# Kernel optimization log

Hardware: AMD Instinct MI355X
Metric: run time of the kernel (lower is better)

The kernel has to match this reference:

```python
import jax, jax.numpy as jnp
import numpy as np
import math

B, NK, NQ = 8, 2048, 2048
DK = DQ = DV = 256
H = 1024


def setup_inputs() -> dict:
    key = jax.random.key(0)
    ks = jax.random.split(key, 11)
    def lin(kw, kb, fan_in, fan_out):
        bound = 1.0 / math.sqrt(fan_in)
        W = jax.random.uniform(kw, (fan_out, fan_in), minval=-bound, maxval=bound, dtype=jnp.float32)
        b = jax.random.uniform(kb, (fan_out,), minval=-bound, maxval=bound, dtype=jnp.float32)
        return W, b
    Wk_w, Wk_b = lin(ks[0], ks[1], DK, H)
    Wq_w, Wq_b = lin(ks[2], ks[3], DQ, H)
    Wv_w, Wv_b = lin(ks[4], ks[5], DV, H)
    lin_w, lin_b = lin(ks[6], ks[7], H, DV)
    KEY = jax.random.normal(ks[8], (B, NK, DK), dtype=jnp.float32)
    VALUE = jax.random.normal(ks[9], (B, NK, DV), dtype=jnp.float32)
    QUERY = jax.random.normal(ks[10], (B, NQ, DQ), dtype=jnp.float32)
    return {"KEY": KEY, "VALUE": VALUE, "QUERY": QUERY,
            "Wk_w": Wk_w, "Wk_b": Wk_b, "Wq_w": Wq_w, "Wq_b": Wq_b,
            "Wv_w": Wv_w, "Wv_b": Wv_b, "lin_w": lin_w, "lin_b": lin_b}


def reference(KEY, VALUE, QUERY, Wk_w, Wk_b, Wq_w, Wq_b, Wv_w, Wv_b, lin_w, lin_b):
    # Projections (dropout in eval mode == identity)
    Wk = KEY @ Wk_w.T + Wk_b      # [b, nk, h]
    Wq = QUERY @ Wq_w.T + Wq_b    # [b, nq, h]
    Wv = VALUE @ Wv_w.T + Wv_b    # [b, nk, h]
    scale = 1.0 / math.sqrt(Wq.shape[-1])
    # dist[b, i(key), k(query)]
    dist = jnp.einsum('bih,bkh->bik', Wk, Wq) * scale
    # softmax over the QUERY axis (dim=2), non-standard
    weights = jax.nn.softmax(dist, axis=2)
    # context[b, k(query), h]
    context = jnp.einsum('bik,bih->bkh', weights, Wv)
    res = context @ lin_w.T + lin_b  # [b, nq, input_v]
    return res
```

## Files before the change

### kernel.cpp

```cpp
#include <hip/hip_runtime.h>
#include <hip/hip_bf16.h>

using bf16 = __hip_bfloat16;
typedef __attribute__((ext_vector_type(8))) short s16x8;
typedef __attribute__((ext_vector_type(4))) float f32x4;

__device__ __forceinline__ void async_cp16(const void* g, void* lds) {
    __builtin_amdgcn_global_load_lds(
        (const __attribute__((address_space(1))) unsigned int*)g,
        (__attribute__((address_space(3))) unsigned int*)lds,
        16, 0, 0);
}

__device__ __forceinline__ void storeC(float* p, float v) { *p = v; }
__device__ __forceinline__ void storeC(bf16* p, float v) { *p = __float2bfloat16(v); }

__device__ __forceinline__ s16x8 pack8(float4 a, float4 b) {
    union { bf16 h[8]; s16x8 v; } o;
    o.h[0] = __float2bfloat16(a.x); o.h[1] = __float2bfloat16(a.y);
    o.h[2] = __float2bfloat16(a.z); o.h[3] = __float2bfloat16(a.w);
    o.h[4] = __float2bfloat16(b.x); o.h[5] = __float2bfloat16(b.y);
    o.h[6] = __float2bfloat16(b.z); o.h[7] = __float2bfloat16(b.w);
    return o.v;
}

__global__ __launch_bounds__(256) void prep_kernel(
    const float* __restrict__ Wk_w, const float* __restrict__ Wk_b,
    const float* __restrict__ Wq_w,
    const float* __restrict__ Wv_w, const float* __restrict__ Wv_b,
    const float* __restrict__ lin_w,
    bf16* __restrict__ WkT, bf16* __restrict__ WqT, bf16* __restrict__ WvT,
    bf16* __restrict__ linb, float* __restrict__ csm)
{
    const int t = threadIdx.x, b = blockIdx.x, y = blockIdx.y;
    if (y <= 2) {
        const float* src = (y == 0) ? Wk_w : (y == 1) ? Wq_w : Wv_w;
        const float* bia = (y == 0) ? Wk_b : Wv_b;
        bf16* dst = (y == 0) ? WkT : (y == 1) ? WqT : WvT;
        if (b < 64) {
            __shared__ float T[64][65];
            const int h0 = (b & 15) * 64, d0 = (b >> 4) * 64;
            const int r = t >> 2, cg = t & 3;
            const float* sp = src + (h0 + r) * 256 + d0 + cg * 16;
#pragma unroll
            for (int c4 = 0; c4 < 4; ++c4) {
                float4 v = *(const float4*)(sp + c4 * 4);
                const int cb = cg * 16 + c4 * 4;
                T[cb + 0][r] = v.x; T[cb + 1][r] = v.y;
                T[cb + 2][r] = v.z; T[cb + 3][r] = v.w;
            }
            __syncthreads();
            union { bf16 h[16]; uint4 u[2]; } o;
#pragma unroll
            for (int j = 0; j < 16; ++j) o.h[j] = __float2bfloat16(T[r][cg * 16 + j]);
            uint4* dp = (uint4*)(dst + (size_t)(d0 + r) * 1024 + h0 + cg * 16);
            dp[0] = o.u[0]; dp[1] = o.u[1];
        } else if (y != 1) {
            if (b < 68) {
                const int i = (b - 64) * 256 + t;
                dst[256 * 1024 + i] = __float2bfloat16(bia[i]);
            } else if (b < 132) {
                const int i = (b - 68) * 256 + t;
                if (i < 127 * 1024 / 8)
                    ((uint4*)(dst + 257 * 1024))[i] = uint4{0, 0, 0, 0};
            }
        }
    } else if (y == 3) {
        const int i = b * 256 + t;
        float4 v = ((const float4*)lin_w)[i];
        union { bf16 h[4]; uint2 u; } o;
        o.h[0] = __float2bfloat16(v.x); o.h[1] = __float2bfloat16(v.y);
        o.h[2] = __float2bfloat16(v.z); o.h[3] = __float2bfloat16(v.w);
        ((uint2*)linb)[i] = o.u;
    } else {
        const int i = b * 256 + t;
        if (i < 4096) ((float4*)csm)[i] = float4{0.f, 0.f, 0.f, 0.f};
    }
}

template <typename OutT, int BIAS, int BN, int SWZ = 0, int EXP = 0, int CVT = 0,
          int CSDIV = 0, int TM = 4>
__global__ __launch_bounds__(256) void gemm_nt(
    const void* __restrict__ Av, const void* __restrict__ Bv,
    OutT* __restrict__ C, const float* __restrict__ bias, int bstride,
    float* __restrict__ colsum,
    int M, int N, int K, int ldA, int ldB,
    long long sA, long long sB, long long sC,
    float scale, int nz, int npn)
{
    constexpr int NF = BN / 32;
    constexpr int BM = TM * 32;
    constexpr bool AF = (CVT & 1) != 0, BF = (CVT & 2) != 0;
    static_assert(!EXP || (AF && BN == 128 && TM == 4), "EXP epilogue layout");
    __shared__ __align__(16) char AsRaw[AF ? BM * 64 * 4 : BM * 64 * 2];
    __shared__ __align__(16) char BsRaw[BF ? BN * 64 * 4 : BN * 64 * 2];
    bf16*  As  = (bf16*)AsRaw;   float* Asf = (float*)AsRaw;
    bf16*  Bs  = (bf16*)BsRaw;   float* Bsf = (float*)BsRaw;

    int bz, m0, n0;
    if constexpr (SWZ) {
        const int bid = blockIdx.x;
        bz = bid % nz;
        const int t0 = bid / nz;
        const int grp = t0 / (4 * npn);
        m0 = (grp * 4 + (t0 % 4)) * BM;
        n0 = ((t0 / 4) % npn) * BN;
    } else {
        bz = blockIdx.z;
        m0 = blockIdx.y * BM;
        n0 = blockIdx.x * BN;
    }
    C += sC * bz;

    const bf16*  A16 = nullptr; const float* A32 = nullptr;
    const bf16*  B16 = nullptr; const float* B32 = nullptr;
    if constexpr (AF) A32 = (const float*)Av + sA * bz;
    else              A16 = (const bf16*)Av + sA * bz;
    if constexpr (BF) B32 = (const float*)Bv + sB * bz;
    else              B16 = (const bf16*)Bv + sB * bz;

    const int t = threadIdx.x;
    const int lane = t & 63;
    const int w = t >> 6;
    const int wm = (w >> 1) * (BM / 2);
    const int wn = (w & 1) * (BN / 2);

    f32x4 acc[TM][NF] = {};

    const int trow = t >> 3;
    const int tcol = (t & 7) ^ (trow & 7);
    const int t16r = t >> 4;
    const int t16c = (t & 15) ^ t16r;
    char* stA = (char*)AsRaw + (size_t)w * 1024;
    char* stB = (char*)BsRaw + (size_t)w * 1024;

    for (int k0 = 0; k0 < K; k0 += 64) {
        __syncthreads();
        if constexpr (AF) {
            const float* a_src = A32 + (long long)(m0 + t16r) * ldA + k0 + t16c * 4;
#pragma unroll
            for (int c = 0; c < BM / 16; ++c)
                async_cp16(a_src + (long long)(c * 16) * ldA, stA + c * 4096);
        } else {
            const bf16* a_src = A16 + (long long)(m0 + trow) * ldA + k0 + tcol * 8;
#pragma unroll
            for (int c = 0; c < BM / 32; ++c)
                async_cp16(a_src + (long long)(c * 32) * ldA, stA + c * 4096);
        }
        if constexpr (BF) {
            const float* b_src = B32 + (long long)(n0 + t16r) * ldB + k0 + t16c * 4;
#pragma unroll
            for (int c = 0; c < BN / 16; ++c)
                async_cp16(b_src + (long long)(c * 16) * ldB, stB + c * 4096);
        } else {
            const bf16* b_src = B16 + (long long)(n0 + trow) * ldB + k0 + tcol * 8;
#pragma unroll
            for (int c = 0; c < NF; ++c)
                async_cp16(b_src + (long long)(c * 32) * ldB, stB + c * 4096);
        }
        __syncthreads();

        const int rl = lane & 15;
        const int quad = lane >> 4;
        const int sw = rl & 7;
#pragma unroll
        for (int kk = 0; kk < 64; kk += 32) {
            const int c8 = (kk >> 3) + quad;
            const int ko = ((c8 ^ sw) << 3);
            const int l0 = (kk >> 2) + quad * 2;
            s16x8 af[TM], bfr[NF];
#pragma unroll
            for (int i = 0; i < TM; ++i) {
                if constexpr (AF) {
                    const float* rp = Asf + (size_t)(wm + i * 16 + rl) * 64;
                    float4 f0 = *(const float4*)(rp + ((l0 ^ rl) << 2));
                    float4 f1 = *(const float4*)(rp + (((l0 + 1) ^ rl) << 2));
                    af[i] = pack8(f0, f1);
                } else {
                    af[i] = *(const s16x8*)(As + (wm + i * 16 + rl) * 64 + ko);
                }
            }
#pragma unroll
            for (int j = 0; j < NF; ++j) {
                if constexpr (BF) {
                    const float* rp = Bsf + (size_t)(wn + j * 16 + rl) * 64;
                    float4 f0 = *(const float4*)(rp + ((l0 ^ rl) << 2));
                    float4 f1 = *(const float4*)(rp + (((l0 + 1) ^ rl) << 2));
                    bfr[j] = pack8(f0, f1);
                } else {
                    bfr[j] = *(const s16x8*)(Bs + (wn + j * 16 + rl) * 64 + ko);
                }
            }
#pragma unroll
            for (int i = 0; i < TM; ++i)
#pragma unroll
                for (int j = 0; j < NF; ++j)
                    acc[i][j] = __builtin_amdgcn_mfma_f32_16x16x32_bf16(
                        af[i], bfr[j], acc[i][j], 0, 0, 0);
        }
    }

    const int cl = lane & 15;
    const int rquad = (lane >> 4) << 2;
    if constexpr (EXP) {
#pragma unroll
        for (int tn = 0; tn < NF; ++tn) {
            const int col = n0 + wn + tn * 16 + cl;
            float csum = 0.f;
#pragma unroll
            for (int tm = 0; tm < TM; ++tm) {
#pragma unroll
                for (int r = 0; r < 4; ++r) {
                    float v = __expf(acc[tm][tn][r] * scale);
                    acc[tm][tn][r] = v;
                    csum += v;
                }
            }
            csum += __shfl_xor(csum, 16);
            csum += __shfl_xor(csum, 32);
            if ((lane >> 4) == 0)
                atomicAdd(&colsum[(long long)bz * N + col], csum);
        }
        float* Ls = (float*)AsRaw;
        const int srow = t >> 3;
        const int scol = (t & 7) * 16;
        const int grb = m0 + ((srow & 16) ? (BM / 2) : 0) + (srow & 15);
#pragma unroll
        for (int tm = 0; tm < TM; ++tm) {
            __syncthreads();
#pragma unroll
            for (int tn = 0; tn < NF; ++tn)
#pragma unroll
                for (int r = 0; r < 4; ++r)
                    Ls[((w >> 1) * 16 + rquad + r) * 132 + wn + tn * 16 + cl] =
                        acc[tm][tn][r];
            __syncthreads();
            float4 f0 = *(const float4*)&Ls[srow * 132 + scol];
            float4 f1 = *(const float4*)&Ls[srow * 132 + scol + 4];
            float4 f2 = *(const float4*)&Ls[srow * 132 + scol + 8];
            float4 f3 = *(const float4*)&Ls[srow * 132 + scol + 12];
            union { s16x8 v; uint4 u; } p0, p1;
            p0.v = pack8(f0, f1);  p1.v = pack8(f2, f3);
            uint4* dst = (uint4*)((bf16*)C + (long long)(grb + tm * 16) * N + n0 + scol);
            dst[0] = p0.u;
            dst[1] = p1.u;
        }
    } else {
#pragma unroll
        for (int tn = 0; tn < NF; ++tn) {
            const int col = n0 + wn + tn * 16 + cl;
            float bcol = 0.f;
            if constexpr (BIAS == 1) bcol = bias[(long long)col * bstride];
            float inv = 1.0f;
            if constexpr (CSDIV == 1) inv = 1.0f / colsum[(long long)bz * N + col];
#pragma unroll
            for (int tm = 0; tm < TM; ++tm) {
#pragma unroll
                for (int r = 0; r < 4; ++r) {
                    const int row = m0 + wm + tm * 16 + rquad + r;
                    float v = acc[tm][tn][r] * scale;
                    if constexpr (BIAS == 1) v += bcol;
                    if constexpr (BIAS == 2) v += bias[(long long)row * bstride];
                    if constexpr (CSDIV == 1) v *= inv;
                    storeC(C + (long long)row * N + col, v);
                }
            }
        }
    }
}

extern "C" void kernel_launch(void* const* d_in, const int* in_sizes, int n_in,
                              void* d_out, int out_size, void* d_ws, size_t ws_size,
                              hipStream_t stream)
{
    constexpr int Bb = 8, NK = 2048, NQ = 2048, D = 256, H = 1024;
    const float scale = 0.03125f;
    constexpr size_t ES  = (size_t)NK * NQ;
    constexpr size_t ET  = (size_t)Bb * NK * D;
    constexpr size_t FIX = 2 * ET * 2
                         + (size_t)512 * 768 * 4
                         + (size_t)512 * 1024 * 2
                         + (size_t)768 * 1024 * 2
                         + (size_t)8 * NK * 4 + 1024;

    const float* KEY   = (const float*)d_in[0];
    const float* VALUE = (const float*)d_in[1];
    const float* QUERY = (const float*)d_in[2];
    const float* Wk_w  = (const float*)d_in[3];
    const float* Wk_b  = (const float*)d_in[4];
    const float* Wq_w  = (const float*)d_in[5];
    const float* Wq_b  = (const float*)d_in[6];
    const float* Wv_w  = (const float*)d_in[7];
    const float* Wv_b  = (const float*)d_in[8];
    const float* lin_w = (const float*)d_in[9];
    const float* lin_b = (const float*)d_in[10];
    float* out = (float*)d_out;
    (void)Wq_b; (void)in_sizes; (void)n_in; (void)out_size;

    auto need = [&](int g) -> size_t { return FIX + (size_t)g * ES * 2; };
    const int g = (ws_size >= need(8)) ? 8 : (ws_size >= need(4)) ? 4 : 2;

    char* ws = (char*)d_ws;
    bf16* Sg   = (bf16*)ws;  ws += (size_t)g * ES * 2;
    bf16* Tp   = (bf16*)ws;  ws += ET * 2;
    bf16* UnT  = (bf16*)ws;  ws += ET * 2;
    float* Cbig= (float*)ws; ws += (size_t)512 * 768 * 4;
    bf16* Abig = (bf16*)ws;  ws += (size_t)512 * 1024 * 2;
    bf16* Bbig = (bf16*)ws;  ws += (size_t)768 * 1024 * 2;
    float* csm = (float*)ws; ws += (size_t)8 * NK * 4;
    bf16* WqT  = Abig;
    bf16* linb = Abig + (size_t)256 * 1024;
    bf16* WkT  = Bbig;
    bf16* WvT  = Bbig + (size_t)384 * 1024;
    const float* C1  = Cbig;
    const float* M2  = Cbig + (size_t)256 * 768 + 384;
    const float* vq  = Cbig + 256;
    const float* c2  = Cbig + (size_t)256 * 768 + 640;

    dim3 blk(256);

    prep_kernel<<<dim3(256, 5), blk, 0, stream>>>(
        Wk_w, Wk_b, Wq_w, Wv_w, Wv_b, lin_w, WkT, WqT, WvT, linb, csm);

    gemm_nt<float, 0, 128><<<dim3(6, 4, 1), blk, 0, stream>>>(
        Abig, Bbig, Cbig, nullptr, 1, nullptr, 512, 768, 1024, 1024, 1024,
        0, 0, 0, 1.0f, 1, 1);

    gemm_nt<bf16, 1, 64, 1, 0, 3, 0, 2><<<dim3(1024), blk, 0, stream>>>(
        KEY, C1, Tp, vq, 768, nullptr, Bb * NK, D, D, D, 768,
        0, 0, 0, 1.0f, 1, 4);

    for (int b0 = 0; b0 < Bb; b0 += g) {
        gemm_nt<bf16, 0, 128, 1, 1, 1, 1, 4><<<dim3(g * (NQ / 128) * (NK / 128)), blk, 0, stream>>>(
            QUERY + (size_t)b0 * NQ * D, Tp + (size_t)b0 * NK * D, Sg,
            nullptr, 1, csm + (size_t)b0 * NK,
            NQ, NK, D, D, D,
            (long long)NQ * D, (long long)NK * D, (long long)NQ * NK, scale,
            g, NK / 128);
        gemm_nt<bf16, 2, 64, 1, 0, 3, 1, 2><<<dim3((g * NK / 64) * 4), blk, 0, stream>>>(
            M2, VALUE + (size_t)b0 * NK * D, UnT,
            c2, 768, csm + (size_t)b0 * NK,
            256, g * NK, D, 768, D,
            0, 0, 0, 1.0f, 1, g * NK / 64);
        gemm_nt<float, 1, 64, 1, 0, 0, 0, 2><<<dim3(g * (NQ / 64) * (D / 64)), blk, 0, stream>>>(
            Sg, UnT, out + (size_t)b0 * NQ * D,
            lin_b, 1, nullptr,
            NQ, D, NK, NK, g * NK,
            (long long)NQ * NK, (long long)NK, (long long)NQ * D, 1.0f,
            g, D / 64);
    }
}
```

Measured before the change: 217.3 us.

## Split-K the weight-product GEMM with atomics and deepen K tile for final GEMM

```diff
diff --git a/kernel.cpp b/kernel.cpp
--- a/kernel.cpp
+++ b/kernel.cpp
@@ -30,7 +30,7 @@
     const float* __restrict__ Wv_w, const float* __restrict__ Wv_b,
     const float* __restrict__ lin_w,
     bf16* __restrict__ WkT, bf16* __restrict__ WqT, bf16* __restrict__ WvT,
-    bf16* __restrict__ linb, float* __restrict__ csm)
+    bf16* __restrict__ linb, float* __restrict__ csm, float* __restrict__ Cbig)
 {
     const int t = threadIdx.x, b = blockIdx.x, y = blockIdx.y;
     if (y <= 2) {
@@ -67,19 +67,22 @@
         }
     } else if (y == 3) {
         const int i = b * 256 + t;
-        float4 v = ((const float4*)lin_w)[i];
-        union { bf16 h[4]; uint2 u; } o;
-        o.h[0] = __float2bfloat16(v.x); o.h[1] = __float2bfloat16(v.y);
-        o.h[2] = __float2bfloat16(v.z); o.h[3] = __float2bfloat16(v.w);
-        ((uint2*)linb)[i] = o.u;
+        if (i < 65536) {
+            float4 v = ((const float4*)lin_w)[i];
+            union { bf16 h[4]; uint2 u; } o;
+            o.h[0] = __float2bfloat16(v.x); o.h[1] = __float2bfloat16(v.y);
+            o.h[2] = __float2bfloat16(v.z); o.h[3] = __float2bfloat16(v.w);
+            ((uint2*)linb)[i] = o.u;
+        }
     } else {
         const int i = b * 256 + t;
         if (i < 4096) ((float4*)csm)[i] = float4{0.f, 0.f, 0.f, 0.f};
+        if (i < 98304) ((float4*)Cbig)[i] = float4{0.f, 0.f, 0.f, 0.f};
     }
 }
 
 template <typename OutT, int BIAS, int BN, int SWZ = 0, int EXP = 0, int CVT = 0,
-          int CSDIV = 0, int TM = 4>
+          int CSDIV = 0, int TM = 4, int BK = 64, int ATOM = 0>
 __global__ __launch_bounds__(256) void gemm_nt(
     const void* __restrict__ Av, const void* __restrict__ Bv,
     OutT* __restrict__ C, const float* __restrict__ bias, int bstride,
@@ -91,9 +94,13 @@
     constexpr int NF = BN / 32;
     constexpr int BM = TM * 32;
     constexpr bool AF = (CVT & 1) != 0, BF = (CVT & 2) != 0;
-    static_assert(!EXP || (AF && BN == 128 && TM == 4), "EXP epilogue layout");
-    __shared__ __align__(16) char AsRaw[AF ? BM * 64 * 4 : BM * 64 * 2];
-    __shared__ __align__(16) char BsRaw[BF ? BN * 64 * 4 : BN * 64 * 2];
+    constexpr int NC8 = BK / 8;
+    constexpr int NC4 = BK / 4;
+    constexpr int RPC8 = 256 / NC8;
+    constexpr int RPC4 = 256 / NC4;
+    static_assert(!EXP || (AF && BN == 128 && TM == 4 && BK == 64), "EXP layout");
+    __shared__ __align__(16) char AsRaw[AF ? BM * BK * 4 : BM * BK * 2];
+    __shared__ __align__(16) char BsRaw[BF ? BN * BK * 4 : BN * BK * 2];
     bf16*  As  = (bf16*)AsRaw;   float* Asf = (float*)AsRaw;
     bf16*  Bs  = (bf16*)BsRaw;   float* Bsf = (float*)BsRaw;
 
@@ -127,68 +134,68 @@
 
     f32x4 acc[TM][NF] = {};
 
-    const int trow = t >> 3;
-    const int tcol = (t & 7) ^ (trow & 7);
-    const int t16r = t >> 4;
-    const int t16c = (t & 15) ^ t16r;
+    const int trow = t / NC8;
+    const int tcol = (t % NC8) ^ (trow % NC8);
+    const int t4r = t / NC4;
+    const int t4c = (t % NC4) ^ (t4r % NC4);
     char* stA = (char*)AsRaw + (size_t)w * 1024;
     char* stB = (char*)BsRaw + (size_t)w * 1024;
 
-    for (int k0 = 0; k0 < K; k0 += 64) {
+    for (int k0 = 0; k0 < K; k0 += BK) {
         __syncthreads();
         if constexpr (AF) {
-            const float* a_src = A32 + (long long)(m0 + t16r) * ldA + k0 + t16c * 4;
-#pragma unroll
-            for (int c = 0; c < BM / 16; ++c)
-                async_cp16(a_src + (long long)(c * 16) * ldA, stA + c * 4096);
+            const float* a_src = A32 + (long long)(m0 + t4r) * ldA + k0 + t4c * 4;
+#pragma unroll
+            for (int c = 0; c < BM / RPC4; ++c)
+                async_cp16(a_src + (long long)(c * RPC4) * ldA, stA + c * 4096);
         } else {
             const bf16* a_src = A16 + (long long)(m0 + trow) * ldA + k0 + tcol * 8;
 #pragma unroll
-            for (int c = 0; c < BM / 32; ++c)
-                async_cp16(a_src + (long long)(c * 32) * ldA, stA + c * 4096);
+            for (int c = 0; c < BM / RPC8; ++c)
+                async_cp16(a_src + (long long)(c * RPC8) * ldA, stA + c * 4096);
         }
         if constexpr (BF) {
-            const float* b_src = B32 + (long long)(n0 + t16r) * ldB + k0 + t16c * 4;
-#pragma unroll
-            for (int c = 0; c < BN / 16; ++c)
-                async_cp16(b_src + (long long)(c * 16) * ldB, stB + c * 4096);
+            const float* b_src = B32 + (long long)(n0 + t4r) * ldB + k0 + t4c * 4;
+#pragma unroll
+            for (int c = 0; c < BN / RPC4; ++c)
+                async_cp16(b_src + (long long)(c * RPC4) * ldB, stB + c * 4096);
         } else {
             const bf16* b_src = B16 + (long long)(n0 + trow) * ldB + k0 + tcol * 8;
 #pragma unroll
-            for (int c = 0; c < NF; ++c)
-                async_cp16(b_src + (long long)(c * 32) * ldB, stB + c * 4096);
+            for (int c = 0; c < BN / RPC8; ++c)
+                async_cp16(b_src + (long long)(c * RPC8) * ldB, stB + c * 4096);
         }
         __syncthreads();
 
         const int rl = lane & 15;
         const int quad = lane >> 4;
-        const int sw = rl & 7;
-#pragma unroll
-        for (int kk = 0; kk < 64; kk += 32) {
+#pragma unroll
+        for (int kk = 0; kk < BK; kk += 32) {
             const int c8 = (kk >> 3) + quad;
-            const int ko = ((c8 ^ sw) << 3);
+            const int ko = ((c8 ^ (rl & (NC8 - 1))) << 3);
             const int l0 = (kk >> 2) + quad * 2;
+            const int k4 = rl & (NC4 - 1);
             s16x8 af[TM], bfr[NF];
 #pragma unroll
             for (int i = 0; i < TM; ++i) {
                 if constexpr (AF) {
-                    const float* rp = Asf + (size_t)(wm + i * 16 + rl) * 64;
-                    float4 f0 = *(const float4*)(rp + ((l0 ^ rl) << 2));
-                    float4 f1 = *(const float4*)(rp + (((l0 + 1) ^ rl) << 2));
+                    const float* rp = Asf + (size_t)(wm + i * 16 + rl) * BK;
+                    float4 f0 = *(const float4*)(rp + ((l0 ^ k4) << 2));
+                    float4 f1 = *(const float4*)(rp + (((l0 + 1) ^ k4) << 2));
                     af[i] = pack8(f0, f1);
                 } else {
-                    af[i] = *(const s16x8*)(As + (wm + i * 16 + rl) * 64 + ko);
+                    af[i] = *(const s16x8*)(As + (size_t)(wm + i * 16 + rl) * BK + ko);
                 }
             }
 #pragma unroll
             for (int j = 0; j < NF; ++j) {
                 if constexpr (BF) {
-                    const float* rp = Bsf + (size_t)(wn + j * 16 + rl) * 64;
-                    float4 f0 = *(const float4*)(rp + ((l0 ^ rl) << 2));
-                    float4 f1 = *(const float4*)(rp + (((l0 + 1) ^ rl) << 2));
+                    const float* rp = Bsf + (size_t)(wn + j * 16 + rl) * BK;
+                    float4 f0 = *(const float4*)(rp + ((l0 ^ k4) << 2));
+                    float4 f1 = *(const float4*)(rp + (((l0 + 1) ^ k4) << 2));
                     bfr[j] = pack8(f0, f1);
                 } else {
-                    bfr[j] = *(const s16x8*)(Bs + (wn + j * 16 + rl) * 64 + ko);
+                    bfr[j] = *(const s16x8*)(Bs + (size_t)(wn + j * 16 + rl) * BK + ko);
                 }
             }
 #pragma unroll
@@ -262,7 +269,10 @@
                     if constexpr (BIAS == 1) v += bcol;
                     if constexpr (BIAS == 2) v += bias[(long long)row * bstride];
                     if constexpr (CSDIV == 1) v *= inv;
-                    storeC(C + (long long)row * N + col, v);
+                    if constexpr (ATOM)
+                        atomicAdd((float*)C + (long long)row * N + col, v);
+                    else
+                        storeC(C + (long long)row * N + col, v);
                 }
             }
         }
@@ -319,12 +329,12 @@
 
     dim3 blk(256);
 
-    prep_kernel<<<dim3(256, 5), blk, 0, stream>>>(
-        Wk_w, Wk_b, Wq_w, Wv_w, Wv_b, lin_w, WkT, WqT, WvT, linb, csm);
-
-    gemm_nt<float, 0, 128><<<dim3(6, 4, 1), blk, 0, stream>>>(
-        Abig, Bbig, Cbig, nullptr, 1, nullptr, 512, 768, 1024, 1024, 1024,
-        0, 0, 0, 1.0f, 1, 1);
+    prep_kernel<<<dim3(384, 5), blk, 0, stream>>>(
+        Wk_w, Wk_b, Wq_w, Wv_w, Wv_b, lin_w, WkT, WqT, WvT, linb, csm, Cbig);
+
+    gemm_nt<float, 0, 128, 0, 0, 0, 0, 4, 64, 1><<<dim3(6, 4, 4), blk, 0, stream>>>(
+        Abig, Bbig, Cbig, nullptr, 1, nullptr, 512, 768, 256, 1024, 1024,
+        256, 256, 0, 1.0f, 1, 1);
 
     gemm_nt<bf16, 1, 64, 1, 0, 3, 0, 2><<<dim3(1024), blk, 0, stream>>>(
         KEY, C1, Tp, vq, 768, nullptr, Bb * NK, D, D, D, 768,
@@ -342,7 +352,7 @@
             c2, 768, csm + (size_t)b0 * NK,
             256, g * NK, D, 768, D,
             0, 0, 0, 1.0f, 1, g * NK / 64);
-        gemm_nt<float, 1, 64, 1, 0, 0, 0, 2><<<dim3(g * (NQ / 64) * (D / 64)), blk, 0, stream>>>(
+        gemm_nt<float, 1, 64, 1, 0, 0, 0, 2, 128><<<dim3(g * (NQ / 64) * (D / 64)), blk, 0, stream>>>(
             Sg, UnT, out + (size_t)b0 * NQ * D,
             lin_b, 1, nullptr,
             NQ, D, NK, NK, g * NK,
```

Result: faster. 213.1 us (-2.0%).
